# Kernel tuning notes

Hardware: AMD Instinct MI355X
Metric: run time of the kernel (lower is better)

## Reference

```python
import jax, jax.numpy as jnp
import numpy as np

B, L, V = 8192, 64, 28
LATENT = 32
PAD_TOKEN, EOS_TOKEN = 26, 27
EPS = 1e-7
LETTER_FREQS = jnp.array([0.0817, 0.0149, 0.0278, 0.0425, 0.127, 0.0223, 0.0202,
                          0.0609, 0.0697, 0.0015, 0.0077, 0.0403, 0.0241, 0.0675,
                          0.0751, 0.0193, 0.001, 0.0599, 0.0633, 0.0906, 0.0276,
                          0.0098, 0.0236, 0.0015, 0.0197, 0.0007], dtype=jnp.float32)
FREQS_PAD = jnp.pad(LETTER_FREQS, (0, V - 26))  # tf.pad to VOCAB_SIZE


def setup_inputs() -> dict:
    key = jax.random.key(0)
    k1, k2, k3, k4, k5 = jax.random.split(key, 5)
    x = jax.random.normal(k1, (B, L, V), dtype=jnp.float32)
    # decoder output is a softmax -> valid probability tensor
    reconstruction = jax.nn.softmax(jax.random.normal(k2, (B, L, V), dtype=jnp.float32), axis=-1)
    z_mean = jax.random.normal(k3, (B, LATENT), dtype=jnp.float32)
    z_log_var = jax.random.normal(k4, (B, LATENT), dtype=jnp.float32)
    classifier_score = jax.random.uniform(k5, (B, 1), dtype=jnp.float32)
    return {"x": x, "reconstruction": reconstruction, "z_mean": z_mean,
            "z_log_var": z_log_var, "classifier_score": classifier_score}


def _total_loss(x, reconstruction, z_mean, z_log_var, classifier_score):
    targets = jnp.argmax(x, axis=-1)                       # [B, L] int
    mask = (targets != PAD_TOKEN).astype(jnp.float32)      # [B, L]

    # sparse categorical CE on probabilities (tf clips probs)
    p_tgt = jnp.take_along_axis(reconstruction, targets[..., None], axis=-1)[..., 0]
    per_position_loss = -jnp.log(jnp.clip(p_tgt, EPS, 1.0))
    reconstruction_loss = jnp.sum(per_position_loss * mask) / jnp.sum(mask)

    kl_loss = -0.5 * jnp.mean(1.0 + z_log_var - jnp.square(z_mean) - jnp.exp(z_log_var))

    classifier_loss = -jnp.mean(jnp.log(classifier_score + EPS))

    # consecutive similarity: sum_i i^2.5 * sum_j prod(adjacent[:, j:j+i])
    mask_adj = (targets[:, 1:] != PAD_TOKEN).astype(jnp.float32)       # [B, L-1]
    adjacent = jnp.sum(reconstruction[:, 1:] * reconstruction[:, :-1], axis=-1) * mask_adj
    Lm1 = L - 1
    pos = jnp.arange(Lm1)

    def step(carry, k):
        # k = i - 1; p[:, j] holds prod(adjacent[:, j:j+k]) from previous step
        p, acc = carry
        valid = (pos < (Lm1 - k)).astype(adjacent.dtype)               # [L-1]
        shifted = jnp.roll(adjacent, -k, axis=1) * valid               # adjacent[:, j+k], 0 past end
        p = p * shifted                                                # window length k+1; invalid j -> 0
        w = jnp.power((k + 1).astype(jnp.float32), 2.5)
        acc = acc + w * jnp.sum(p)
        return (p, acc), None

    init = (adjacent, jnp.sum(adjacent))                               # i = 1, weight 1^2.5
    (_, consecutive_similarity), _ = jax.lax.scan(step, init, jnp.arange(1, Lm1))

    mask_exp = jnp.logical_and(targets != PAD_TOKEN, targets != EOS_TOKEN).astype(jnp.float32)[:, :, None]
    mean_letter_probs = jnp.sum(reconstruction * mask_exp, axis=(0, 1)) / jnp.sum(mask_exp)
    frequency_penalty = jnp.sum(jnp.maximum(0.0, mean_letter_probs - FREQS_PAD))

    total_loss = (reconstruction_loss + 0.1 * kl_loss + 2.0 * classifier_loss
                  + 0.2 * consecutive_similarity + 0.5 * frequency_penalty)
    return total_loss


def reference(x, reconstruction, z_mean, z_log_var, classifier_score):
    return _total_loss(x, reconstruction, z_mean, z_log_var, classifier_score)
```

## Files before the change

kernel.cpp:

```cpp
#include <hip/hip_runtime.h>
#include <math.h>

#define VB 28
#define LL 64
#define PAD_TOK 26
#define EOS_TOK 27

__device__ __forceinline__ float wave_red(float v) {
  #pragma unroll
  for (int o = 32; o > 0; o >>= 1) v += __shfl_down(v, o, 64);
  return v;
}

__global__ __launch_bounds__(256) void vae_main(const float* __restrict__ x,
                                                const float* __restrict__ rec,
                                                float* __restrict__ ws,
                                                int nrows) {
  __shared__ float w_pow[64];
  __shared__ float red[4][32];
  const int lane = threadIdx.x & 63;
  const int wid  = threadIdx.x >> 6;
  if (threadIdx.x < 63) w_pow[threadIdx.x] = powf((float)(threadIdx.x + 1), 2.5f);
  __syncthreads();

  float loss_acc = 0.f, mask_cnt = 0.f, consec_acc = 0.f, mexp_cnt = 0.f;
  float vocab[VB];
  #pragma unroll
  for (int v = 0; v < VB; ++v) vocab[v] = 0.f;

  const int wave_id = blockIdx.x * 4 + wid;
  const int n_waves = gridDim.x * 4;

  for (int row = wave_id; row < nrows; row += n_waves) {
    const size_t base = ((size_t)row * LL + lane) * VB;
    const float4* xp = reinterpret_cast<const float4*>(x + base);
    const float4* rp = reinterpret_cast<const float4*>(rec + base);
    float r[VB];
    float best = -INFINITY, pt = 0.f;
    int tgt = 0;
    #pragma unroll
    for (int i = 0; i < 7; ++i) {
      float4 xq = xp[i];
      float4 rq = rp[i];
      r[i*4+0] = rq.x; r[i*4+1] = rq.y; r[i*4+2] = rq.z; r[i*4+3] = rq.w;
      if (xq.x > best) { best = xq.x; tgt = i*4+0; pt = rq.x; }
      if (xq.y > best) { best = xq.y; tgt = i*4+1; pt = rq.y; }
      if (xq.z > best) { best = xq.z; tgt = i*4+2; pt = rq.z; }
      if (xq.w > best) { best = xq.w; tgt = i*4+3; pt = rq.w; }
    }
    const float mask = (tgt != PAD_TOK) ? 1.f : 0.f;
    const float mexp = (tgt != PAD_TOK && tgt != EOS_TOK) ? 1.f : 0.f;
    loss_acc += -logf(fminf(fmaxf(pt, 1e-7f), 1.f)) * mask;
    mask_cnt += mask;
    mexp_cnt += mexp;
    #pragma unroll
    for (int v = 0; v < VB; ++v) vocab[v] += r[v] * mexp;

    float adj = 0.f;
    #pragma unroll
    for (int v = 0; v < VB; ++v) adj += r[v] * __shfl_down(r[v], 1, 64);
    const int tgt_next = __shfl_down(tgt, 1, 64);
    adj = (lane < 63 && tgt_next != PAD_TOK) ? adj : 0.f;

    float p = adj;
    consec_acc += p;
    for (int k = 1; k < 63; ++k) {
      const float sh = __shfl_down(adj, k, 64);
      p = (lane < 63 - k) ? p * sh : 0.f;
      consec_acc += w_pow[k] * p;
      if (__ballot(p != 0.f) == 0ull) break;
    }
  }

  loss_acc   = wave_red(loss_acc);
  mask_cnt   = wave_red(mask_cnt);
  consec_acc = wave_red(consec_acc);
  mexp_cnt   = wave_red(mexp_cnt);
  #pragma unroll
  for (int v = 0; v < VB; ++v) vocab[v] = wave_red(vocab[v]);

  if (lane == 0) {
    red[wid][0] = loss_acc;
    red[wid][1] = mask_cnt;
    red[wid][2] = consec_acc;
    red[wid][3] = mexp_cnt;
    #pragma unroll
    for (int v = 0; v < VB; ++v) red[wid][4 + v] = vocab[v];
  }
  __syncthreads();
  if (threadIdx.x < 32) {
    const int j = threadIdx.x;
    const float s = red[0][j] + red[1][j] + red[2][j] + red[3][j];
    const int dst = (j < 4) ? j : (6 + (j - 4));
    atomicAdd(&ws[dst], s);
  }
}

__global__ __launch_bounds__(256) void vae_klcls(const float* __restrict__ zm,
                                                 const float* __restrict__ zlv,
                                                 const float* __restrict__ cs,
                                                 float* __restrict__ ws,
                                                 int nz, int nc) {
  __shared__ float red[4][2];
  const int lane = threadIdx.x & 63;
  const int wid  = threadIdx.x >> 6;
  const int gid = blockIdx.x * blockDim.x + threadIdx.x;
  const int stride = gridDim.x * blockDim.x;
  float kl = 0.f, cl = 0.f;
  for (int i = gid; i < nz; i += stride) {
    const float m = zm[i], lv = zlv[i];
    kl += 1.f + lv - m * m - expf(lv);
  }
  for (int i = gid; i < nc; i += stride) cl += logf(cs[i] + 1e-7f);
  kl = wave_red(kl);
  cl = wave_red(cl);
  if (lane == 0) { red[wid][0] = kl; red[wid][1] = cl; }
  __syncthreads();
  if (threadIdx.x < 2) {
    const float s = red[0][threadIdx.x] + red[1][threadIdx.x] +
                    red[2][threadIdx.x] + red[3][threadIdx.x];
    atomicAdd(&ws[4 + threadIdx.x], s);
  }
}

__global__ void vae_finalize(const float* __restrict__ ws, float* __restrict__ out,
                             float nz, float nc) {
  if (threadIdx.x == 0 && blockIdx.x == 0) {
    const float freqs[VB] = {0.0817f,0.0149f,0.0278f,0.0425f,0.127f,0.0223f,0.0202f,
      0.0609f,0.0697f,0.0015f,0.0077f,0.0403f,0.0241f,0.0675f,0.0751f,0.0193f,0.001f,
      0.0599f,0.0633f,0.0906f,0.0276f,0.0098f,0.0236f,0.0015f,0.0197f,0.0007f,0.f,0.f};
    const float rec_loss = ws[0] / ws[1];
    const float kl       = -0.5f * ws[4] / nz;
    const float cls      = -ws[5] / nc;
    const float inv_mexp = 1.f / ws[3];
    float fp = 0.f;
    #pragma unroll
    for (int v = 0; v < VB; ++v) fp += fmaxf(0.f, ws[6 + v] * inv_mexp - freqs[v]);
    out[0] = rec_loss + 0.1f * kl + 2.f * cls + 0.2f * ws[2] + 0.5f * fp;
  }
}

extern "C" void kernel_launch(void* const* d_in, const int* in_sizes, int n_in,
                              void* d_out, int out_size, void* d_ws, size_t ws_size,
                              hipStream_t stream) {
  const float* x   = (const float*)d_in[0];
  const float* rec = (const float*)d_in[1];
  const float* zm  = (const float*)d_in[2];
  const float* zlv = (const float*)d_in[3];
  const float* cs  = (const float*)d_in[4];
  float* out = (float*)d_out;
  float* ws  = (float*)d_ws;

  const int nz    = in_sizes[2];
  const int nc    = in_sizes[4];
  const int nrows = in_sizes[0] / (LL * VB);

  hipMemsetAsync(d_ws, 0, 64 * sizeof(float), stream);
  vae_main<<<1024, 256, 0, stream>>>(x, rec, ws, nrows);
  vae_klcls<<<128, 256, 0, stream>>>(zm, zlv, cs, ws, nz, nc);
  vae_finalize<<<1, 64, 0, stream>>>(ws, out, (float)nz, (float)nc);
}
```

Before: 170.3 us.

## Fuse main, KL/classifier and finalize kernels into one last-block-reduce kernel

Merges the three kernels into a single launch. The KL and classifier sums are computed inside the main kernel, and the last block to finish does the final reduction, chosen through an atomic counter. Atomics are spread across 8 replicated workspace banks to cut contention. The grid now has one wave per row (2048 blocks), the consecutive-product loop is unrolled by 8 with an early-exit ballot per chunk, and fast intrinsics (__logf, __expf, __powf) are used. This removes launch overhead and tail serialization, but the fast math may shift the result slightly.

```diff
diff --git a/kernel.cpp b/kernel.cpp
--- a/kernel.cpp
+++ b/kernel.cpp
@@ -5,6 +5,9 @@
 #define LL 64
 #define PAD_TOK 26
 #define EOS_TOK 27
+#define NSLOT 34
+#define REPL 8
+#define CNT_IDX 512
 
 __device__ __forceinline__ float wave_red(float v) {
   #pragma unroll
@@ -12,15 +15,20 @@
   return v;
 }
 
-__global__ __launch_bounds__(256) void vae_main(const float* __restrict__ x,
-                                                const float* __restrict__ rec,
-                                                float* __restrict__ ws,
-                                                int nrows) {
-  __shared__ float w_pow[64];
-  __shared__ float red[4][32];
+__global__ __launch_bounds__(256) void vae_fused(
+    const float* __restrict__ x, const float* __restrict__ rec,
+    const float* __restrict__ zm, const float* __restrict__ zlv,
+    const float* __restrict__ cs, float* __restrict__ ws,
+    float* __restrict__ out, int nrows, int nz, int nc, int nblocks) {
+  __shared__ float w_pow[72];
+  __shared__ float red[4][NSLOT];
+  __shared__ float fin[NSLOT];
+  __shared__ int last_flag;
   const int lane = threadIdx.x & 63;
   const int wid  = threadIdx.x >> 6;
-  if (threadIdx.x < 63) w_pow[threadIdx.x] = powf((float)(threadIdx.x + 1), 2.5f);
+  if (threadIdx.x < 72)
+    w_pow[threadIdx.x] = (threadIdx.x < 62)
+        ? __powf((float)(threadIdx.x + 1), 2.5f) : 0.f;
   __syncthreads();
 
   float loss_acc = 0.f, mask_cnt = 0.f, consec_acc = 0.f, mexp_cnt = 0.f;
@@ -29,7 +37,7 @@
   for (int v = 0; v < VB; ++v) vocab[v] = 0.f;
 
   const int wave_id = blockIdx.x * 4 + wid;
-  const int n_waves = gridDim.x * 4;
+  const int n_waves = nblocks * 4;
 
   for (int row = wave_id; row < nrows; row += n_waves) {
     const size_t base = ((size_t)row * LL + lane) * VB;
@@ -50,7 +58,7 @@
     }
     const float mask = (tgt != PAD_TOK) ? 1.f : 0.f;
     const float mexp = (tgt != PAD_TOK && tgt != EOS_TOK) ? 1.f : 0.f;
-    loss_acc += -logf(fminf(fmaxf(pt, 1e-7f), 1.f)) * mask;
+    loss_acc += -__logf(fminf(fmaxf(pt, 1e-7f), 1.f)) * mask;
     mask_cnt += mask;
     mexp_cnt += mexp;
     #pragma unroll
@@ -64,79 +72,85 @@
 
     float p = adj;
     consec_acc += p;
-    for (int k = 1; k < 63; ++k) {
-      const float sh = __shfl_down(adj, k, 64);
-      p = (lane < 63 - k) ? p * sh : 0.f;
-      consec_acc += w_pow[k] * p;
+    #pragma unroll 1
+    for (int k0 = 1; k0 < 62; k0 += 8) {
+      #pragma unroll
+      for (int u = 0; u < 8; ++u) {
+        const int k = k0 + u;
+        float sh = __shfl(adj, lane + k, 64);
+        sh = (k <= 61 && lane + k <= 62) ? sh : 0.f;
+        p *= sh;
+        consec_acc += w_pow[k] * p;
+      }
       if (__ballot(p != 0.f) == 0ull) break;
     }
   }
+
+  const int gid = blockIdx.x * 256 + threadIdx.x;
+  const int gstride = nblocks * 256;
+  float kl = 0.f, cl = 0.f;
+  for (int i = gid; i < nz; i += gstride) {
+    const float m = zm[i], lv = zlv[i];
+    kl += 1.f + lv - m * m - __expf(lv);
+  }
+  for (int i = gid; i < nc; i += gstride) cl += __logf(cs[i] + 1e-7f);
 
   loss_acc   = wave_red(loss_acc);
   mask_cnt   = wave_red(mask_cnt);
   consec_acc = wave_red(consec_acc);
   mexp_cnt   = wave_red(mexp_cnt);
+  kl         = wave_red(kl);
+  cl         = wave_red(cl);
   #pragma unroll
   for (int v = 0; v < VB; ++v) vocab[v] = wave_red(vocab[v]);
 
   if (lane == 0) {
-    red[wid][0] = loss_acc;
-    red[wid][1] = mask_cnt;
-    red[wid][2] = consec_acc;
-    red[wid][3] = mexp_cnt;
+    red[wid][0] = loss_acc; red[wid][1] = mask_cnt;
+    red[wid][2] = consec_acc; red[wid][3] = mexp_cnt;
+    red[wid][4] = kl; red[wid][5] = cl;
     #pragma unroll
-    for (int v = 0; v < VB; ++v) red[wid][4 + v] = vocab[v];
+    for (int v = 0; v < VB; ++v) red[wid][6 + v] = vocab[v];
   }
   __syncthreads();
-  if (threadIdx.x < 32) {
-    const int j = threadIdx.x;
-    const float s = red[0][j] + red[1][j] + red[2][j] + red[3][j];
-    const int dst = (j < 4) ? j : (6 + (j - 4));
-    atomicAdd(&ws[dst], s);
+
+  float* bank = ws + ((blockIdx.x & (REPL - 1)) << 6);
+  if (threadIdx.x < NSLOT) {
+    const int t = threadIdx.x;
+    atomicAdd(&bank[t], red[0][t] + red[1][t] + red[2][t] + red[3][t]);
   }
-}
+  __threadfence();
+  __syncthreads();
+  if (threadIdx.x == 0) {
+    unsigned old = atomicAdd(reinterpret_cast<unsigned*>(ws + CNT_IDX), 1u);
+    last_flag = (old == (unsigned)(nblocks - 1)) ? 1 : 0;
+  }
+  __syncthreads();
 
-__global__ __launch_bounds__(256) void vae_klcls(const float* __restrict__ zm,
-                                                 const float* __restrict__ zlv,
-                                                 const float* __restrict__ cs,
-                                                 float* __restrict__ ws,
-                                                 int nz, int nc) {
-  __shared__ float red[4][2];
-  const int lane = threadIdx.x & 63;
-  const int wid  = threadIdx.x >> 6;
-  const int gid = blockIdx.x * blockDim.x + threadIdx.x;
-  const int stride = gridDim.x * blockDim.x;
-  float kl = 0.f, cl = 0.f;
-  for (int i = gid; i < nz; i += stride) {
-    const float m = zm[i], lv = zlv[i];
-    kl += 1.f + lv - m * m - expf(lv);
-  }
-  for (int i = gid; i < nc; i += stride) cl += logf(cs[i] + 1e-7f);
-  kl = wave_red(kl);
-  cl = wave_red(cl);
-  if (lane == 0) { red[wid][0] = kl; red[wid][1] = cl; }
-  __syncthreads();
-  if (threadIdx.x < 2) {
-    const float s = red[0][threadIdx.x] + red[1][threadIdx.x] +
-                    red[2][threadIdx.x] + red[3][threadIdx.x];
-    atomicAdd(&ws[4 + threadIdx.x], s);
-  }
-}
-
-__global__ void vae_finalize(const float* __restrict__ ws, float* __restrict__ out,
-                             float nz, float nc) {
-  if (threadIdx.x == 0 && blockIdx.x == 0) {
-    const float freqs[VB] = {0.0817f,0.0149f,0.0278f,0.0425f,0.127f,0.0223f,0.0202f,
-      0.0609f,0.0697f,0.0015f,0.0077f,0.0403f,0.0241f,0.0675f,0.0751f,0.0193f,0.001f,
-      0.0599f,0.0633f,0.0906f,0.0276f,0.0098f,0.0236f,0.0015f,0.0197f,0.0007f,0.f,0.f};
-    const float rec_loss = ws[0] / ws[1];
-    const float kl       = -0.5f * ws[4] / nz;
-    const float cls      = -ws[5] / nc;
-    const float inv_mexp = 1.f / ws[3];
-    float fp = 0.f;
-    #pragma unroll
-    for (int v = 0; v < VB; ++v) fp += fmaxf(0.f, ws[6 + v] * inv_mexp - freqs[v]);
-    out[0] = rec_loss + 0.1f * kl + 2.f * cls + 0.2f * ws[2] + 0.5f * fp;
+  if (last_flag) {
+    if (threadIdx.x < NSLOT) {
+      float tot = 0.f;
+      #pragma unroll
+      for (int rp2 = 0; rp2 < REPL; ++rp2)
+        tot += atomicAdd(&ws[(rp2 << 6) + threadIdx.x], 0.f);
+      fin[threadIdx.x] = tot;
+    }
+    __syncthreads();
+    if (threadIdx.x == 0) {
+      const float freqs[VB] = {0.0817f,0.0149f,0.0278f,0.0425f,0.127f,0.0223f,
+        0.0202f,0.0609f,0.0697f,0.0015f,0.0077f,0.0403f,0.0241f,0.0675f,0.0751f,
+        0.0193f,0.001f,0.0599f,0.0633f,0.0906f,0.0276f,0.0098f,0.0236f,0.0015f,
+        0.0197f,0.0007f,0.f,0.f};
+      const float rec_loss = fin[0] / fin[1];
+      const float kl_loss  = -0.5f * fin[4] / (float)nz;
+      const float cls_loss = -fin[5] / (float)nc;
+      const float inv_mexp = 1.f / fin[3];
+      float fp = 0.f;
+      #pragma unroll
+      for (int v = 0; v < VB; ++v)
+        fp += fmaxf(0.f, fin[6 + v] * inv_mexp - freqs[v]);
+      out[0] = rec_loss + 0.1f * kl_loss + 2.f * cls_loss
+             + 0.2f * fin[2] + 0.5f * fp;
+    }
   }
 }
 
@@ -151,12 +165,14 @@
   float* out = (float*)d_out;
   float* ws  = (float*)d_ws;
 
+  const int nrows = in_sizes[0] / (LL * VB);
   const int nz    = in_sizes[2];
   const int nc    = in_sizes[4];
-  const int nrows = in_sizes[0] / (LL * VB);
 
-  hipMemsetAsync(d_ws, 0, 64 * sizeof(float), stream);
-  vae_main<<<1024, 256, 0, stream>>>(x, rec, ws, nrows);
-  vae_klcls<<<128, 256, 0, stream>>>(zm, zlv, cs, ws, nz, nc);
-  vae_finalize<<<1, 64, 0, stream>>>(ws, out, (float)nz, (float)nc);
+  int nblocks = (nrows + 3) / 4;
+  if (nblocks < 1) nblocks = 1;
+
+  hipMemsetAsync(d_ws, 0, (CNT_IDX + 4) * sizeof(float), stream);
+  vae_fused<<<nblocks, 256, 0, stream>>>(x, rec, zm, zlv, cs, ws, out,
+                                         nrows, nz, nc, nblocks);
 }
```

Measured after the change: 443.0 us. 160% more time.
